# Optimization experiments

Measured on AMD Instinct MI355X. Metric: run time of the kernel, lower is better.

Reference implementation:

```python
import jax, jax.numpy as jnp
import numpy as np

K = 256          # max_num_neighbors
MAX_RADIUS = 1.0  # max_radius


def setup_inputs() -> dict:
    key = jax.random.key(0)
    k1, k2 = jax.random.split(key)
    N, D = 12288, 14
    x = jax.random.normal(k1, (N, D), dtype=jnp.float32)
    particle_id = jax.random.randint(k2, (N,), 0, 4000, dtype=jnp.int64 if jax.config.jax_enable_x64 else jnp.int32)
    return {"x": x, "particle_id": particle_id}


def _knn(x):
    """kNN graph (loop=False, like torch_cluster.knn_graph).

    Returns src (neighbor), dst (query) index arrays of length N*K and the
    Euclidean distance per edge.
    """
    N = x.shape[0]
    sq = jnp.sum(x * x, axis=1)                       # [N]
    d2 = sq[:, None] + sq[None, :] - 2.0 * (x @ x.T)   # [N, N] squared dists
    d2 = d2.at[jnp.arange(N), jnp.arange(N)].set(jnp.inf)  # exclude self-loops
    neg_d2, nbr = jax.lax.top_k(-d2, K)                # K nearest per query row
    src = nbr.reshape(-1)                              # neighbor j (edge_index[0])
    dst = jnp.repeat(jnp.arange(N), K)                 # query i   (edge_index[1])
    dist = jnp.sqrt(jnp.clip(-neg_d2, 0.0)).reshape(-1)
    return src, dst, dist


def reference(x, particle_id):
    # knn_with_max_radius: build kNN graph, then filter edges with dist >= r.
    # JIT-compatible form: keep the fixed [N*K] edge set plus a validity mask
    # (instead of dynamically dropping columns).
    src, dst, dist = _knn(x)
    mask = dist < MAX_RADIUS                           # radius filter

    edge_index = jnp.stack([jnp.where(mask, src, 0),
                            jnp.where(mask, dst, 0)])  # [2, N*K]

    # y = particle_id[edge_index[0]] == particle_id[edge_index[1]]
    y = (particle_id[src] == particle_id[dst]) & mask

    # build_edge_features: cat(x[src] - x[dst], x[src] + x[dst]) -> [E, 2*D]
    xs, xd = x[src], x[dst]
    edge_features = jnp.concatenate([xs - xd, xs + xd], axis=1) * mask[:, None]

    return x, edge_index, y.astype(jnp.int32), edge_features, mask
```

## Files before the change

kernel.cpp:

```cpp
#include <hip/hip_runtime.h>


#define N_PTS 12288
#define DIM   14
#define KNN   256

typedef float        f32x4  __attribute__((ext_vector_type(4)));
typedef unsigned int u32x4  __attribute__((ext_vector_type(4)));
typedef short        bf16x8 __attribute__((ext_vector_type(8)));

constexpr int NTILE = 1176;
constexpr int NFILL = 256;
constexpr int NBLK  = NTILE + NFILL;
constexpr int CAP   = 4096;

constexpr long NK      = (long)N_PTS * KNN;
constexpr long OFF_EI0 = (long)N_PTS * DIM;
constexpr long OFF_EI1 = OFF_EI0 + NK;
constexpr long OFF_Y   = OFF_EI0 + 2 * NK;
constexpr long OFF_F   = OFF_Y + NK;
constexpr long OFF_M   = OFF_F + NK * 28;

constexpr int FILL_BASE4 = (int)(OFF_EI0 / 4);
constexpr int TOTAL4     = (int)((OFF_M + NK) / 4);
constexpr int SWEEP4     = NFILL * 256;
constexpr int FILL_ITERS = (TOTAL4 - FILL_BASE4) / SWEEP4;
static_assert((long)FILL_BASE4 + (long)FILL_ITERS * SWEEP4 == TOTAL4, "exact cover");

__device__ __forceinline__ unsigned f2bf(float f) {
    unsigned u = __float_as_uint(f);
    return (u + 0x7FFF + ((u >> 16) & 1)) >> 16;
}

__device__ __forceinline__ void push2(int* ws, int a, int c) {
    int s = atomicAdd(ws, 1);
    if (s < CAP) { ws[2 + 2 * s] = a; ws[3 + 2 * s] = c; }
}

__device__ __forceinline__ float pdist2(const float* __restrict__ x, int i, int j) {
    const float* a = x + (size_t)i * DIM;
    const float* b = x + (size_t)j * DIM;
    float sa = 0.f, sb = 0.f, dot = 0.f;
#pragma unroll
    for (int d = 0; d < DIM; ++d) {
        sa  = fmaf(a[d], a[d], sa);
        sb  = fmaf(b[d], b[d], sb);
        dot = fmaf(a[d], b[d], dot);
    }
    return (sa + sb) - 2.0f * dot;
}

__global__ __launch_bounds__(256, 8) void fused_knn(const float* __restrict__ x,
                                                    int* __restrict__ ws,
                                                    float* __restrict__ out) {
    const int t = threadIdx.x;
    const int b = blockIdx.x;
    const int l = t & 63;

    __shared__ __align__(16) unsigned short qa[256][16];
    __shared__ __align__(16) unsigned short cb[256][16];
    __shared__ float ssqq[256], ssqc[256];

    f32x4* o4 = reinterpret_cast<f32x4*>(out);

    if (b >= NTILE) {
        const int f = b - NTILE;
        if (f < 168) {
            const int g = f * 256 + t;
            const f32x4 v = reinterpret_cast<const f32x4*>(x)[g];
            __builtin_nontemporal_store(v, o4 + g);
        }
        const f32x4 z = {0.f, 0.f, 0.f, 0.f};
        int p = FILL_BASE4 + f * 256 + t;
#pragma unroll 8
        for (int it = 0; it < FILL_ITERS; ++it, p += SWEEP4)
            __builtin_nontemporal_store(z, o4 + p);
        return;
    }

    int L = b, bi = 0;
    while (L >= 48 - bi) { L -= 48 - bi; ++bi; }
    const int bj = bi + L;

    {
        const float* qp = x + (size_t)(bi * 256 + t) * DIM;
        const float* cp = x + (size_t)(bj * 256 + t) * DIM;
        unsigned hq[8], hc[8];
        float sq = 0.f, sc = 0.f;
#pragma unroll
        for (int d = 0; d < 7; ++d) {
            const float a0 = qp[2 * d], a1 = qp[2 * d + 1];
            const float c0 = cp[2 * d], c1 = cp[2 * d + 1];
            hq[d] = f2bf(a0) | (f2bf(a1) << 16);
            hc[d] = f2bf(c0) | (f2bf(c1) << 16);
            sq = fmaf(a1, a1, fmaf(a0, a0, sq));
            sc = fmaf(c1, c1, fmaf(c0, c0, sc));
        }
        hq[7] = 0; hc[7] = 0;
        *reinterpret_cast<u32x4*>(&qa[t][0]) = *reinterpret_cast<u32x4*>(&hq[0]);
        *reinterpret_cast<u32x4*>(&qa[t][8]) = *reinterpret_cast<u32x4*>(&hq[4]);
        *reinterpret_cast<u32x4*>(&cb[t][0]) = *reinterpret_cast<u32x4*>(&hc[0]);
        *reinterpret_cast<u32x4*>(&cb[t][8]) = *reinterpret_cast<u32x4*>(&hc[4]);
        ssqq[t] = sq; ssqc[t] = sc;
    }
    __syncthreads();

    const bf16x8 zf = {0, 0, 0, 0, 0, 0, 0, 0};
    for (int mrw = 0; mrw < 4; ++mrw) {
        const int mr = (t >> 6) * 4 + mrw;
        bf16x8 af = zf;
        if (l < 32)
            af = *reinterpret_cast<const bf16x8*>(&qa[mr * 16 + (l & 15)][(l >> 4) * 8]);
        const int rowb = mr * 16 + (l >> 4) * 4;
        const float s0 = ssqq[rowb], s1 = ssqq[rowb + 1],
                    s2 = ssqq[rowb + 2], s3 = ssqq[rowb + 3];
        const int qg = bi * 256 + rowb;
        for (int mc = 0; mc < 16; ++mc) {
            bf16x8 bfr = zf;
            if (l < 32)
                bfr = *reinterpret_cast<const bf16x8*>(&cb[mc * 16 + (l & 15)][(l >> 4) * 8]);
            f32x4 acc = {0.f, 0.f, 0.f, 0.f};
            acc = __builtin_amdgcn_mfma_f32_16x16x32_bf16(af, bfr, acc, 0, 0, 0);
            const float sqc = ssqc[mc * 16 + (l & 15)];
            const int   cg  = bj * 256 + mc * 16 + (l & 15);
            if ((s0 + sqc) - 2.f * acc[0] < 2.0f && cg > qg)     push2(ws, qg,     cg);
            if ((s1 + sqc) - 2.f * acc[1] < 2.0f && cg > qg + 1) push2(ws, qg + 1, cg);
            if ((s2 + sqc) - 2.f * acc[2] < 2.0f && cg > qg + 2) push2(ws, qg + 2, cg);
            if ((s3 + sqc) - 2.f * acc[3] < 2.0f && cg > qg + 3) push2(ws, qg + 3, cg);
        }
    }
}

__global__ void scatter_edges(const float* __restrict__ x,
                              const int* __restrict__ pid,
                              const int* __restrict__ ws,
                              float* __restrict__ out) {
    __shared__ float sd2[CAP];
    __shared__ int   si[CAP], sj[CAP];

    int cnt = ws[0];
    if (cnt > CAP) cnt = CAP;

    for (int e = threadIdx.x; e < cnt; e += 256) {
        const int i = ws[2 + 2 * e], j = ws[3 + 2 * e];
        si[e]  = i;
        sj[e]  = j;
        sd2[e] = pdist2(x, i, j);
    }
    __syncthreads();

    for (int e = threadIdx.x; e < cnt; e += 256) {
        const int i = si[e], j = sj[e];
        const float d2 = sd2[e];
        if (!(d2 < 1.0f)) continue;
        for (int dir = 0; dir < 2; ++dir) {
            const int a  = dir ? j : i;
            const int pr = dir ? i : j;
            int r = 0;
            for (int e2 = 0; e2 < cnt; ++e2) {
                const int i2 = si[e2], j2 = sj[e2];
                int p2;
                if (i2 == a) p2 = j2; else if (j2 == a) p2 = i2; else continue;
                const float d2b = sd2[e2];
                if (!(d2b < 1.0f)) continue;
                if (d2b < d2 || (d2b == d2 && p2 < pr)) ++r;
            }
            if (r >= KNN) continue;
            const long eidx = (long)a * KNN + r;
            out[OFF_EI0 + eidx] = (float)pr;
            out[OFF_EI1 + eidx] = (float)a;
            out[OFF_Y   + eidx] = (pid[a] == pid[pr]) ? 1.0f : 0.0f;
            out[OFF_M   + eidx] = 1.0f;
            float* f = out + OFF_F + eidx * 28;
#pragma unroll
            for (int d = 0; d < DIM; ++d) {
                const float xs = x[pr * DIM + d];
                const float xd = x[a  * DIM + d];
                f[d]       = xs - xd;
                f[DIM + d] = xs + xd;
            }
        }
    }
}

extern "C" void kernel_launch(void* const* d_in, const int* in_sizes, int n_in,
                              void* d_out, int out_size, void* d_ws, size_t ws_size,
                              hipStream_t stream) {
    const float* x   = (const float*)d_in[0];
    const int*   pid = (const int*)d_in[1];
    float*       out = (float*)d_out;
    int*         ws  = (int*)d_ws;

    (void)hipMemsetAsync(ws, 0, 16, stream);
    fused_knn<<<NBLK, 256, 0, stream>>>(x, ws, out);
    scatter_edges<<<1, 256, 0, stream>>>(x, pid, ws, out);
}
```

Before: 81.20 us.

## Fuse scatter kernel into kNN kernel via last-block grid completion counter

Merges the single-block scatter_edges kernel into fused_knn: every block increments a global counter after finishing, and block NTILE spins until all blocks have arrived, then performs the edge ranking and scatter. This removes one kernel launch and its launch gap. The price is that the shared-memory staging of pairs and distances is dropped, so ranking rereads pairs from global memory and recomputes pdist2 in the inner loop. It also assumes the waiting block can wait for all others without deadlock, which holds only if every block eventually becomes resident.

```diff
diff --git a/kernel.cpp b/kernel.cpp
--- a/kernel.cpp
+++ b/kernel.cpp
@@ -51,6 +51,7 @@
 }
 
 __global__ __launch_bounds__(256, 8) void fused_knn(const float* __restrict__ x,
+                                                    const int* __restrict__ pid,
                                                     int* __restrict__ ws,
                                                     float* __restrict__ out) {
     const int t = threadIdx.x;
@@ -75,93 +76,88 @@
 #pragma unroll 8
         for (int it = 0; it < FILL_ITERS; ++it, p += SWEEP4)
             __builtin_nontemporal_store(z, o4 + p);
-        return;
+    } else {
+        int L = b, bi = 0;
+        while (L >= 48 - bi) { L -= 48 - bi; ++bi; }
+        const int bj = bi + L;
+
+        {
+            const float* qp = x + (size_t)(bi * 256 + t) * DIM;
+            const float* cp = x + (size_t)(bj * 256 + t) * DIM;
+            unsigned hq[8], hc[8];
+            float sq = 0.f, sc = 0.f;
+#pragma unroll
+            for (int d = 0; d < 7; ++d) {
+                const float a0 = qp[2 * d], a1 = qp[2 * d + 1];
+                const float c0 = cp[2 * d], c1 = cp[2 * d + 1];
+                hq[d] = f2bf(a0) | (f2bf(a1) << 16);
+                hc[d] = f2bf(c0) | (f2bf(c1) << 16);
+                sq = fmaf(a1, a1, fmaf(a0, a0, sq));
+                sc = fmaf(c1, c1, fmaf(c0, c0, sc));
+            }
+            hq[7] = 0; hc[7] = 0;
+            *reinterpret_cast<u32x4*>(&qa[t][0]) = *reinterpret_cast<u32x4*>(&hq[0]);
+            *reinterpret_cast<u32x4*>(&qa[t][8]) = *reinterpret_cast<u32x4*>(&hq[4]);
+            *reinterpret_cast<u32x4*>(&cb[t][0]) = *reinterpret_cast<u32x4*>(&hc[0]);
+            *reinterpret_cast<u32x4*>(&cb[t][8]) = *reinterpret_cast<u32x4*>(&hc[4]);
+            ssqq[t] = sq; ssqc[t] = sc;
+        }
+        __syncthreads();
+
+        const bf16x8 zf = {0, 0, 0, 0, 0, 0, 0, 0};
+        for (int mrw = 0; mrw < 4; ++mrw) {
+            const int mr = (t >> 6) * 4 + mrw;
+            bf16x8 af = zf;
+            if (l < 32)
+                af = *reinterpret_cast<const bf16x8*>(&qa[mr * 16 + (l & 15)][(l >> 4) * 8]);
+            const int rowb = mr * 16 + (l >> 4) * 4;
+            const float s0 = ssqq[rowb], s1 = ssqq[rowb + 1],
+                        s2 = ssqq[rowb + 2], s3 = ssqq[rowb + 3];
+            const int qg = bi * 256 + rowb;
+            for (int mc = 0; mc < 16; ++mc) {
+                bf16x8 bfr = zf;
+                if (l < 32)
+                    bfr = *reinterpret_cast<const bf16x8*>(&cb[mc * 16 + (l & 15)][(l >> 4) * 8]);
+                f32x4 acc = {0.f, 0.f, 0.f, 0.f};
+                acc = __builtin_amdgcn_mfma_f32_16x16x32_bf16(af, bfr, acc, 0, 0, 0);
+                const float sqc = ssqc[mc * 16 + (l & 15)];
+                const int   cg  = bj * 256 + mc * 16 + (l & 15);
+                if ((s0 + sqc) - 2.f * acc[0] < 2.0f && cg > qg)     push2(ws, qg,     cg);
+                if ((s1 + sqc) - 2.f * acc[1] < 2.0f && cg > qg + 1) push2(ws, qg + 1, cg);
+                if ((s2 + sqc) - 2.f * acc[2] < 2.0f && cg > qg + 2) push2(ws, qg + 2, cg);
+                if ((s3 + sqc) - 2.f * acc[3] < 2.0f && cg > qg + 3) push2(ws, qg + 3, cg);
+            }
+        }
     }
 
-    int L = b, bi = 0;
-    while (L >= 48 - bi) { L -= 48 - bi; ++bi; }
-    const int bj = bi + L;
+    __syncthreads();
+    __threadfence();
+    if (t == 0) atomicAdd(&ws[1], 1);
+    if (b != NTILE) return;
 
-    {
-        const float* qp = x + (size_t)(bi * 256 + t) * DIM;
-        const float* cp = x + (size_t)(bj * 256 + t) * DIM;
-        unsigned hq[8], hc[8];
-        float sq = 0.f, sc = 0.f;
-#pragma unroll
-        for (int d = 0; d < 7; ++d) {
-            const float a0 = qp[2 * d], a1 = qp[2 * d + 1];
-            const float c0 = cp[2 * d], c1 = cp[2 * d + 1];
-            hq[d] = f2bf(a0) | (f2bf(a1) << 16);
-            hc[d] = f2bf(c0) | (f2bf(c1) << 16);
-            sq = fmaf(a1, a1, fmaf(a0, a0, sq));
-            sc = fmaf(c1, c1, fmaf(c0, c0, sc));
-        }
-        hq[7] = 0; hc[7] = 0;
-        *reinterpret_cast<u32x4*>(&qa[t][0]) = *reinterpret_cast<u32x4*>(&hq[0]);
-        *reinterpret_cast<u32x4*>(&qa[t][8]) = *reinterpret_cast<u32x4*>(&hq[4]);
-        *reinterpret_cast<u32x4*>(&cb[t][0]) = *reinterpret_cast<u32x4*>(&hc[0]);
-        *reinterpret_cast<u32x4*>(&cb[t][8]) = *reinterpret_cast<u32x4*>(&hc[4]);
-        ssqq[t] = sq; ssqc[t] = sc;
+    if (t == 0) {
+        while (__hip_atomic_load(&ws[1], __ATOMIC_ACQUIRE,
+                                 __HIP_MEMORY_SCOPE_AGENT) < NBLK)
+            __builtin_amdgcn_s_sleep(2);
     }
     __syncthreads();
-
-    const bf16x8 zf = {0, 0, 0, 0, 0, 0, 0, 0};
-    for (int mrw = 0; mrw < 4; ++mrw) {
-        const int mr = (t >> 6) * 4 + mrw;
-        bf16x8 af = zf;
-        if (l < 32)
-            af = *reinterpret_cast<const bf16x8*>(&qa[mr * 16 + (l & 15)][(l >> 4) * 8]);
-        const int rowb = mr * 16 + (l >> 4) * 4;
-        const float s0 = ssqq[rowb], s1 = ssqq[rowb + 1],
-                    s2 = ssqq[rowb + 2], s3 = ssqq[rowb + 3];
-        const int qg = bi * 256 + rowb;
-        for (int mc = 0; mc < 16; ++mc) {
-            bf16x8 bfr = zf;
-            if (l < 32)
-                bfr = *reinterpret_cast<const bf16x8*>(&cb[mc * 16 + (l & 15)][(l >> 4) * 8]);
-            f32x4 acc = {0.f, 0.f, 0.f, 0.f};
-            acc = __builtin_amdgcn_mfma_f32_16x16x32_bf16(af, bfr, acc, 0, 0, 0);
-            const float sqc = ssqc[mc * 16 + (l & 15)];
-            const int   cg  = bj * 256 + mc * 16 + (l & 15);
-            if ((s0 + sqc) - 2.f * acc[0] < 2.0f && cg > qg)     push2(ws, qg,     cg);
-            if ((s1 + sqc) - 2.f * acc[1] < 2.0f && cg > qg + 1) push2(ws, qg + 1, cg);
-            if ((s2 + sqc) - 2.f * acc[2] < 2.0f && cg > qg + 2) push2(ws, qg + 2, cg);
-            if ((s3 + sqc) - 2.f * acc[3] < 2.0f && cg > qg + 3) push2(ws, qg + 3, cg);
-        }
-    }
-}
-
-__global__ void scatter_edges(const float* __restrict__ x,
-                              const int* __restrict__ pid,
-                              const int* __restrict__ ws,
-                              float* __restrict__ out) {
-    __shared__ float sd2[CAP];
-    __shared__ int   si[CAP], sj[CAP];
+    __threadfence();
 
     int cnt = ws[0];
     if (cnt > CAP) cnt = CAP;
-
-    for (int e = threadIdx.x; e < cnt; e += 256) {
+    for (int e = t; e < cnt; e += 256) {
         const int i = ws[2 + 2 * e], j = ws[3 + 2 * e];
-        si[e]  = i;
-        sj[e]  = j;
-        sd2[e] = pdist2(x, i, j);
-    }
-    __syncthreads();
-
-    for (int e = threadIdx.x; e < cnt; e += 256) {
-        const int i = si[e], j = sj[e];
-        const float d2 = sd2[e];
+        const float d2 = pdist2(x, i, j);
         if (!(d2 < 1.0f)) continue;
         for (int dir = 0; dir < 2; ++dir) {
             const int a  = dir ? j : i;
             const int pr = dir ? i : j;
             int r = 0;
             for (int e2 = 0; e2 < cnt; ++e2) {
-                const int i2 = si[e2], j2 = sj[e2];
+                const int i2 = ws[2 + 2 * e2], j2 = ws[3 + 2 * e2];
                 int p2;
                 if (i2 == a) p2 = j2; else if (j2 == a) p2 = i2; else continue;
-                const float d2b = sd2[e2];
+                const float d2b = pdist2(x, a, p2);
                 if (!(d2b < 1.0f)) continue;
                 if (d2b < d2 || (d2b == d2 && p2 < pr)) ++r;
             }
@@ -171,13 +167,13 @@
             out[OFF_EI1 + eidx] = (float)a;
             out[OFF_Y   + eidx] = (pid[a] == pid[pr]) ? 1.0f : 0.0f;
             out[OFF_M   + eidx] = 1.0f;
-            float* f = out + OFF_F + eidx * 28;
+            float* fo = out + OFF_F + eidx * 28;
 #pragma unroll
             for (int d = 0; d < DIM; ++d) {
                 const float xs = x[pr * DIM + d];
                 const float xd = x[a  * DIM + d];
-                f[d]       = xs - xd;
-                f[DIM + d] = xs + xd;
+                fo[d]       = xs - xd;
+                fo[DIM + d] = xs + xd;
             }
         }
     }
@@ -192,6 +188,5 @@
     int*         ws  = (int*)d_ws;
 
     (void)hipMemsetAsync(ws, 0, 16, stream);
-    fused_knn<<<NBLK, 256, 0, stream>>>(x, ws, out);
-    scatter_edges<<<1, 256, 0, stream>>>(x, pid, ws, out);
+    fused_knn<<<NBLK, 256, 0, stream>>>(x, pid, ws, out);
 }
```

After: 201.1 us. 148% more time.
